# Kernel tuning notes

Measured on AMD Instinct MI355X. Metric: run time of the kernel, lower is better.

The kernel has to match this reference:

```python
import jax, jax.numpy as jnp
import numpy as np

W1 = W2 = W3 = 7  # window size


def _rel_pos_indices(w1, w2, w3):
    # Static relative-position index table, matching the torch buffer.
    g = np.stack(np.meshgrid(np.arange(w1), np.arange(w2), np.arange(w3), indexing='ij'))
    g = g.reshape(3, -1).T                      # (N, 3), N = w1*w2*w3
    rel = g[:, None, :] - g[None, :, :]         # (N, N, 3)
    rel[..., 0] += w1 - 1
    rel[..., 1] += w2 - 1
    rel[..., 2] += w3 - 1
    strides = np.array([(2 * w2 - 1) * (2 * w3 - 1), 2 * w3 - 1, 1])
    return jnp.asarray((rel * strides).sum(-1), dtype=jnp.int32)  # (N, N)


def setup_inputs() -> dict:
    key = jax.random.key(0)
    k1, k2, k3, k4 = jax.random.split(key, 4)
    dim, heads = 256, 8
    x = jax.random.normal(k1, (2, 4, 4, 4, W1, W2, W3, dim), dtype=jnp.float32)
    w_qkv = jax.random.normal(k2, (dim, 3 * dim), dtype=jnp.float32) * (dim ** -0.5)
    w_out = jax.random.normal(k3, (dim, dim), dtype=jnp.float32) * (dim ** -0.5)
    n_rel = (2 * W1 - 1) * (2 * W2 - 1) * (2 * W3 - 1)  # 2197
    rel_bias_table = jax.random.normal(k4, (n_rel, heads), dtype=jnp.float32) * 0.02
    return {"x": x, "w_qkv": w_qkv, "w_out": w_out, "rel_bias_table": rel_bias_table}


def reference(x, w_qkv, w_out, rel_bias_table):
    b, gx, gy, gz, w1, w2, w3, d = x.shape
    heads = rel_bias_table.shape[1]
    dh = d // heads
    scale = dh ** -0.5
    n = w1 * w2 * w3
    B = b * gx * gy * gz

    xf = x.reshape(B, n, d)
    qkv = xf @ w_qkv                             # (B, n, 3d)
    q, k, v = jnp.split(qkv, 3, axis=-1)

    def to_heads(t):
        return t.reshape(B, n, heads, dh).transpose(0, 2, 1, 3)  # (B, h, n, dh)

    q, k, v = to_heads(q), to_heads(k), to_heads(v)

    rel_idx = _rel_pos_indices(w1, w2, w3)                       # (n, n)
    bias = rel_bias_table[rel_idx].transpose(2, 0, 1)            # (h, n, n)

    logits = jnp.einsum('bhnd,bhmd->bhnm', q, k) * scale + bias[None]
    attn = jax.nn.softmax(logits, axis=-1)
    ctx = jnp.einsum('bhnm,bhmd->bhnd', attn, v)                 # (B, h, n, dh)

    out = ctx.transpose(0, 2, 1, 3).reshape(B, n, d) @ w_out     # (B, n, d)
    return out.reshape(b, gx, gy, gz, w1, w2, w3, d)
```

## Files before the change

kernel.cpp:

```cpp
#include <hip/hip_runtime.h>
#include <math.h>

using f16   = _Float16;
using f16x4 = __attribute__((ext_vector_type(4))) _Float16;
using f16x8 = __attribute__((ext_vector_type(8))) _Float16;
using f32x4 = __attribute__((ext_vector_type(4))) float;

#define NW    343
#define NWP   352
#define VTP   356
#define HEADS 8
#define MTOT  43904
#define LOG2E 1.4426950408889634f
#define QSC   (0.17677669529663687f * 1.4426950408889634f)

typedef const __attribute__((address_space(1))) unsigned int* gp1_t;
typedef __attribute__((address_space(3))) unsigned int* lp3_t;
__device__ __forceinline__ void gload_lds16(const void* g, void* l) {
    __builtin_amdgcn_global_load_lds((gp1_t)g, (lp3_t)l, 16, 0, 0);
}

__global__ void cvt_x(const float* __restrict__ x, f16* __restrict__ xb) {
    int id = blockIdx.x * 256 + threadIdx.x;
    float4 v = *(const float4*)(x + id * 4);
    f16x4 o = { (f16)v.x, (f16)v.y, (f16)v.z, (f16)v.w };
    *(f16x4*)(xb + id * 4) = o;
}

__global__ void cvt_wT(const float* __restrict__ W, f16* __restrict__ WT,
                       int N, int scaleN, float sc) {
    int id = blockIdx.x * 256 + threadIdx.x;
    int n = id >> 8, k = id & 255;
    float v = W[k * N + n];
    if (n < scaleN) v *= sc;
    WT[n * 256 + k] = (f16)v;
}

__global__ void bias_k(const float* __restrict__ tab, float* __restrict__ bp) {
    int id = blockIdx.x * 256 + threadIdx.x;
    int h = id / (NWP * NWP);
    int rem = id - h * NWP * NWP;
    int i = rem / NWP, j = rem - (rem / NWP) * NWP;
    float v;
    if (j >= NW) v = -1e30f;
    else if (i >= NW) v = 0.f;
    else {
        int a1 = i / 49, a2 = (i / 7) % 7, a3 = i % 7;
        int b1 = j / 49, b2 = (j / 7) % 7, b3 = j % 7;
        int idx = (a1 - b1 + 6) * 169 + (a2 - b2 + 6) * 13 + (a3 - b3 + 6);
        v = tab[idx * 8 + h] * LOG2E;
    }
    bp[id] = v;
}

template<bool OUT_F32>
__launch_bounds__(256)
__global__ void gemm_k(const f16* __restrict__ A, const f16* __restrict__ Bt,
                       void* __restrict__ Cp, int N) {
    __shared__ f16 As[128 * 32];
    __shared__ f16 Bs[128 * 32];
    const int m0 = blockIdx.x * 128;
    const int n0 = blockIdx.y * 128;
    const int t = threadIdx.x;
    const int wave = t >> 6, lane = t & 63;
    const int q = lane >> 4, c = lane & 15;
    const int wm = (wave >> 1) * 64, wn = (wave & 1) * 64;
    const int r0 = t >> 2;
    const int c8 = (t & 3) * 8;

    f32x4 acc[4][4] = {};
#pragma unroll
    for (int ks = 0; ks < 256; ks += 32) {
        gload_lds16(&A[(size_t)(m0 + r0) * 256 + ks + c8],        &As[r0 * 32 + c8]);
        gload_lds16(&A[(size_t)(m0 + r0 + 64) * 256 + ks + c8],   &As[(r0 + 64) * 32 + c8]);
        gload_lds16(&Bt[(size_t)(n0 + r0) * 256 + ks + c8],       &Bs[r0 * 32 + c8]);
        gload_lds16(&Bt[(size_t)(n0 + r0 + 64) * 256 + ks + c8],  &Bs[(r0 + 64) * 32 + c8]);
        __syncthreads();
        f16x8 af[4], bf[4];
#pragma unroll
        for (int a = 0; a < 4; a++) af[a] = *(const f16x8*)&As[(wm + a * 16 + c) * 32 + q * 8];
#pragma unroll
        for (int b = 0; b < 4; b++) bf[b] = *(const f16x8*)&Bs[(wn + b * 16 + c) * 32 + q * 8];
#pragma unroll
        for (int a = 0; a < 4; a++)
#pragma unroll
            for (int b = 0; b < 4; b++)
                acc[a][b] = __builtin_amdgcn_mfma_f32_16x16x32_f16(af[a], bf[b], acc[a][b], 0, 0, 0);
        __syncthreads();
    }
#pragma unroll
    for (int a = 0; a < 4; a++)
#pragma unroll
        for (int b = 0; b < 4; b++) {
            int row0 = m0 + wm + a * 16 + q * 4;
            int col = n0 + wn + b * 16 + c;
#pragma unroll
            for (int r = 0; r < 4; r++) {
                float v = acc[a][b][r];
                if (OUT_F32) ((float*)Cp)[(size_t)(row0 + r) * N + col] = v;
                else         ((f16*)Cp)[(size_t)(row0 + r) * N + col] = (f16)v;
            }
        }
}

__launch_bounds__(512)
__global__ void attn_k(const f16* __restrict__ qkv, const float* __restrict__ biasP,
                       f16* __restrict__ ctx) {
    const int w = blockIdx.x >> 3;
    const int h = blockIdx.x & 7;
    __shared__ f16 Ks[NWP * 32];
    __shared__ f16 Vt[32 * VTP];
    const int t = threadIdx.x;
    const size_t base = (size_t)(w * NW) * 768;

    for (int u = t; u < NWP * 4; u += 512) {
        int row = u >> 2, un = u & 3;
        uint4 val;
        if (row < NW) val = *(const uint4*)&qkv[base + (size_t)row * 768 + 256 + h * 32 + un * 8];
        else { val.x = val.y = val.z = val.w = 0u; }
        *(uint4*)&Ks[row * 32 + un * 8] = val;
    }
    for (int u = t; u < NWP * 4; u += 512) {
        int row = u >> 2, un = u & 3;
        if (row < NW) {
            uint4 val = *(const uint4*)&qkv[base + (size_t)row * 768 + 512 + h * 32 + un * 8];
            const f16* pv = (const f16*)&val;
#pragma unroll
            for (int e = 0; e < 8; e++) Vt[(un * 8 + e) * VTP + row] = pv[e];
        } else {
#pragma unroll
            for (int e = 0; e < 8; e++) Vt[(un * 8 + e) * VTP + row] = (f16)0.f;
        }
    }
    __syncthreads();

    const int wave = t >> 6, lane = t & 63;
    const int q = lane >> 4, c = lane & 15;
    const float* biasH = biasP + (size_t)h * NWP * NWP;

    for (int qt = wave; qt < NWP / 16; qt += 8) {
        const int iq = qt * 16 + c;
        const int iqc = iq < NW ? iq : NW - 1;
        f16x8 qf = *(const f16x8*)&qkv[base + (size_t)iqc * 768 + h * 32 + q * 8];
        const float* brow = biasH + (size_t)iq * NWP;

        f32x4 o0 = {0.f, 0.f, 0.f, 0.f}, o1 = {0.f, 0.f, 0.f, 0.f};
        float lsum = 0.f;
#pragma unroll
        for (int jt = 0; jt < NWP / 16; jt++) {
            const int jb = jt * 16;
            f16x8 kf = *(const f16x8*)&Ks[(jb + c) * 32 + q * 8];
            f32x4 z = {0.f, 0.f, 0.f, 0.f};
            f32x4 s = __builtin_amdgcn_mfma_f32_16x16x32_f16(kf, qf, z, 0, 0, 0);
            f32x4 b4 = *(const f32x4*)&brow[jb + q * 4];
            float p0 = __builtin_amdgcn_exp2f(s[0] + b4[0]);
            float p1 = __builtin_amdgcn_exp2f(s[1] + b4[1]);
            float p2 = __builtin_amdgcn_exp2f(s[2] + b4[2]);
            float p3 = __builtin_amdgcn_exp2f(s[3] + b4[3]);
            lsum += (p0 + p1) + (p2 + p3);
            f16x4 pf = { (f16)p0, (f16)p1, (f16)p2, (f16)p3 };
            f16x4 v0 = *(const f16x4*)&Vt[c * VTP + jb + q * 4];
            f16x4 v1 = *(const f16x4*)&Vt[(16 + c) * VTP + jb + q * 4];
            o0 = __builtin_amdgcn_mfma_f32_16x16x16f16(v0, pf, o0, 0, 0, 0);
            o1 = __builtin_amdgcn_mfma_f32_16x16x16f16(v1, pf, o1, 0, 0, 0);
        }
        lsum += __shfl_xor(lsum, 16);
        lsum += __shfl_xor(lsum, 32);

        if (iq < NW) {
            float inv = 1.f / lsum;
            size_t ob = (size_t)(w * NW + iq) * 256 + h * 32;
            f16x4 s0 = { (f16)(o0[0] * inv), (f16)(o0[1] * inv),
                         (f16)(o0[2] * inv), (f16)(o0[3] * inv) };
            f16x4 s1 = { (f16)(o1[0] * inv), (f16)(o1[1] * inv),
                         (f16)(o1[2] * inv), (f16)(o1[3] * inv) };
            *(f16x4*)&ctx[ob + q * 4] = s0;
            *(f16x4*)&ctx[ob + 16 + q * 4] = s1;
        }
    }
}

extern "C" void kernel_launch(void* const* d_in, const int* in_sizes, int n_in,
                              void* d_out, int out_size, void* d_ws, size_t ws_size,
                              hipStream_t stream) {
    const float* x    = (const float*)d_in[0];
    const float* wqkv = (const float*)d_in[1];
    const float* wout = (const float*)d_in[2];
    const float* tab  = (const float*)d_in[3];

    char* ws = (char*)d_ws;
    size_t off = 0;
    f16*   xb     = (f16*)(ws + off);   off += (size_t)MTOT * 256 * 2;
    f16*   wqkvT  = (f16*)(ws + off);   off += (size_t)768 * 256 * 2;
    f16*   woutT  = (f16*)(ws + off);   off += (size_t)256 * 256 * 2;
    float* biasP  = (float*)(ws + off); off += (size_t)8 * NWP * NWP * 4;
    f16*   qkvb   = (f16*)(ws + off);   off += (size_t)MTOT * 768 * 2;
    f16*   ctxb   = (f16*)(ws + off);   off += (size_t)MTOT * 256 * 2;
    if (ws_size < off) return;

    cvt_x <<<MTOT * 256 / 1024, 256, 0, stream>>>(x, xb);
    cvt_wT<<<768, 256, 0, stream>>>(wqkv, wqkvT, 768, 256, QSC);
    cvt_wT<<<256, 256, 0, stream>>>(wout, woutT, 256, 0, 1.f);
    bias_k<<<8 * NWP * NWP / 256, 256, 0, stream>>>(tab, biasP);
    gemm_k<false><<<dim3(MTOT / 128, 768 / 128), 256, 0, stream>>>(xb, wqkvT, qkvb, 768);
    attn_k<<<128 * HEADS, 512, 0, stream>>>(qkvb, biasP, ctxb);
    gemm_k<true><<<dim3(MTOT / 128, 256 / 128), 256, 0, stream>>>(ctxb, woutT, d_out, 256);
}
```

Measured before the change: 236.0 us.

## Merge prep kernels, widen GEMM K-tile with swizzle, pad K LDS, split attention accumulators

Three small setup kernels become one launch. The GEMM now stages 64-wide K tiles with an XOR-style swizzle that avoids LDS bank conflicts, which halves the barrier count, and it sets an occupancy hint in launch bounds. In attention, the K rows in LDS are padded to 40, the bias is folded into the QK MFMA accumulator input, and the loop alternates between two accumulator sets to shorten dependency chains. The larger LDS tiles and extra accumulators add register and LDS pressure, which may cost occupancy.

```diff
diff --git a/kernel.cpp b/kernel.cpp
--- a/kernel.cpp
+++ b/kernel.cpp
@@ -8,6 +8,7 @@
 
 #define NW    343
 #define NWP   352
+#define KSP   40
 #define VTP   356
 #define HEADS 8
 #define MTOT  43904
@@ -27,65 +28,81 @@
     *(f16x4*)(xb + id * 4) = o;
 }
 
-__global__ void cvt_wT(const float* __restrict__ W, f16* __restrict__ WT,
-                       int N, int scaleN, float sc) {
-    int id = blockIdx.x * 256 + threadIdx.x;
-    int n = id >> 8, k = id & 255;
-    float v = W[k * N + n];
-    if (n < scaleN) v *= sc;
-    WT[n * 256 + k] = (f16)v;
-}
-
-__global__ void bias_k(const float* __restrict__ tab, float* __restrict__ bp) {
-    int id = blockIdx.x * 256 + threadIdx.x;
-    int h = id / (NWP * NWP);
-    int rem = id - h * NWP * NWP;
-    int i = rem / NWP, j = rem - (rem / NWP) * NWP;
-    float v;
-    if (j >= NW) v = -1e30f;
-    else if (i >= NW) v = 0.f;
-    else {
-        int a1 = i / 49, a2 = (i / 7) % 7, a3 = i % 7;
-        int b1 = j / 49, b2 = (j / 7) % 7, b3 = j % 7;
-        int idx = (a1 - b1 + 6) * 169 + (a2 - b2 + 6) * 13 + (a3 - b3 + 6);
-        v = tab[idx * 8 + h] * LOG2E;
-    }
-    bp[id] = v;
+__global__ void prep_k(const float* __restrict__ wqkv, const float* __restrict__ wout,
+                       const float* __restrict__ tab,
+                       f16* __restrict__ wqkvT, f16* __restrict__ woutT,
+                       float* __restrict__ bp) {
+    int b = blockIdx.x, t = threadIdx.x;
+    if (b < 768) {
+        float v = wqkv[t * 768 + b];
+        if (b < 256) v *= QSC;
+        wqkvT[b * 256 + t] = (f16)v;
+    } else if (b < 1024) {
+        int n = b - 768;
+        woutT[n * 256 + t] = (f16)wout[t * 256 + n];
+    } else {
+        int id = (b - 1024) * 256 + t;
+        int h = id / (NWP * NWP);
+        int rem = id - h * NWP * NWP;
+        int i = rem / NWP, j = rem - (rem / NWP) * NWP;
+        float v;
+        if (j >= NW) v = -1e30f;
+        else if (i >= NW) v = 0.f;
+        else {
+            int a1 = i / 49, a2 = (i / 7) % 7, a3 = i % 7;
+            int b1 = j / 49, b2 = (j / 7) % 7, b3 = j % 7;
+            int idx = (a1 - b1 + 6) * 169 + (a2 - b2 + 6) * 13 + (a3 - b3 + 6);
+            v = tab[idx * 8 + h] * LOG2E;
+        }
+        bp[id] = v;
+    }
 }
 
 template<bool OUT_F32>
-__launch_bounds__(256)
+__launch_bounds__(256, 3)
 __global__ void gemm_k(const f16* __restrict__ A, const f16* __restrict__ Bt,
                        void* __restrict__ Cp, int N) {
-    __shared__ f16 As[128 * 32];
-    __shared__ f16 Bs[128 * 32];
+    __shared__ f16 As[128 * 64];
+    __shared__ f16 Bs[128 * 64];
     const int m0 = blockIdx.x * 128;
     const int n0 = blockIdx.y * 128;
     const int t = threadIdx.x;
     const int wave = t >> 6, lane = t & 63;
     const int q = lane >> 4, c = lane & 15;
     const int wm = (wave >> 1) * 64, wn = (wave & 1) * 64;
-    const int r0 = t >> 2;
-    const int c8 = (t & 3) * 8;
+    const int sr = t >> 3;
+    const int sb = t & 7;
 
     f32x4 acc[4][4] = {};
 #pragma unroll
-    for (int ks = 0; ks < 256; ks += 32) {
-        gload_lds16(&A[(size_t)(m0 + r0) * 256 + ks + c8],        &As[r0 * 32 + c8]);
-        gload_lds16(&A[(size_t)(m0 + r0 + 64) * 256 + ks + c8],   &As[(r0 + 64) * 32 + c8]);
-        gload_lds16(&Bt[(size_t)(n0 + r0) * 256 + ks + c8],       &Bs[r0 * 32 + c8]);
-        gload_lds16(&Bt[(size_t)(n0 + r0 + 64) * 256 + ks + c8],  &Bs[(r0 + 64) * 32 + c8]);
+    for (int ks = 0; ks < 256; ks += 64) {
+#pragma unroll
+        for (int j = 0; j < 4; j++) {
+            int row = j * 32 + sr;
+            int gb = (sb - row) & 7;
+            gload_lds16(&A[(size_t)(m0 + row) * 256 + ks + gb * 8], &As[row * 64 + sb * 8]);
+            gload_lds16(&Bt[(size_t)(n0 + row) * 256 + ks + gb * 8], &Bs[row * 64 + sb * 8]);
+        }
         __syncthreads();
-        f16x8 af[4], bf[4];
-#pragma unroll
-        for (int a = 0; a < 4; a++) af[a] = *(const f16x8*)&As[(wm + a * 16 + c) * 32 + q * 8];
-#pragma unroll
-        for (int b = 0; b < 4; b++) bf[b] = *(const f16x8*)&Bs[(wn + b * 16 + c) * 32 + q * 8];
-#pragma unroll
-        for (int a = 0; a < 4; a++)
-#pragma unroll
-            for (int b = 0; b < 4; b++)
-                acc[a][b] = __builtin_amdgcn_mfma_f32_16x16x32_f16(af[a], bf[b], acc[a][b], 0, 0, 0);
+#pragma unroll
+        for (int ko = 0; ko < 2; ko++) {
+            f16x8 af[4], bf[4];
+#pragma unroll
+            for (int a = 0; a < 4; a++) {
+                int row = wm + a * 16 + c;
+                af[a] = *(const f16x8*)&As[row * 64 + ((ko * 4 + q + row) & 7) * 8];
+            }
+#pragma unroll
+            for (int b = 0; b < 4; b++) {
+                int row = wn + b * 16 + c;
+                bf[b] = *(const f16x8*)&Bs[row * 64 + ((ko * 4 + q + row) & 7) * 8];
+            }
+#pragma unroll
+            for (int a = 0; a < 4; a++)
+#pragma unroll
+                for (int b = 0; b < 4; b++)
+                    acc[a][b] = __builtin_amdgcn_mfma_f32_16x16x32_f16(af[a], bf[b], acc[a][b], 0, 0, 0);
+        }
         __syncthreads();
     }
 #pragma unroll
@@ -103,12 +120,12 @@
         }
 }
 
-__launch_bounds__(512)
+__launch_bounds__(512, 4)
 __global__ void attn_k(const f16* __restrict__ qkv, const float* __restrict__ biasP,
                        f16* __restrict__ ctx) {
     const int w = blockIdx.x >> 3;
     const int h = blockIdx.x & 7;
-    __shared__ f16 Ks[NWP * 32];
+    __shared__ f16 Ks[NWP * KSP];
     __shared__ f16 Vt[32 * VTP];
     const int t = threadIdx.x;
     const size_t base = (size_t)(w * NW) * 768;
@@ -118,7 +135,7 @@
         uint4 val;
         if (row < NW) val = *(const uint4*)&qkv[base + (size_t)row * 768 + 256 + h * 32 + un * 8];
         else { val.x = val.y = val.z = val.w = 0u; }
-        *(uint4*)&Ks[row * 32 + un * 8] = val;
+        *(uint4*)&Ks[row * KSP + un * 8] = val;
     }
     for (int u = t; u < NWP * 4; u += 512) {
         int row = u >> 2, un = u & 3;
@@ -144,36 +161,55 @@
         f16x8 qf = *(const f16x8*)&qkv[base + (size_t)iqc * 768 + h * 32 + q * 8];
         const float* brow = biasH + (size_t)iq * NWP;
 
-        f32x4 o0 = {0.f, 0.f, 0.f, 0.f}, o1 = {0.f, 0.f, 0.f, 0.f};
-        float lsum = 0.f;
-#pragma unroll
-        for (int jt = 0; jt < NWP / 16; jt++) {
-            const int jb = jt * 16;
-            f16x8 kf = *(const f16x8*)&Ks[(jb + c) * 32 + q * 8];
-            f32x4 z = {0.f, 0.f, 0.f, 0.f};
-            f32x4 s = __builtin_amdgcn_mfma_f32_16x16x32_f16(kf, qf, z, 0, 0, 0);
-            f32x4 b4 = *(const f32x4*)&brow[jb + q * 4];
-            float p0 = __builtin_amdgcn_exp2f(s[0] + b4[0]);
-            float p1 = __builtin_amdgcn_exp2f(s[1] + b4[1]);
-            float p2 = __builtin_amdgcn_exp2f(s[2] + b4[2]);
-            float p3 = __builtin_amdgcn_exp2f(s[3] + b4[3]);
-            lsum += (p0 + p1) + (p2 + p3);
-            f16x4 pf = { (f16)p0, (f16)p1, (f16)p2, (f16)p3 };
-            f16x4 v0 = *(const f16x4*)&Vt[c * VTP + jb + q * 4];
-            f16x4 v1 = *(const f16x4*)&Vt[(16 + c) * VTP + jb + q * 4];
-            o0 = __builtin_amdgcn_mfma_f32_16x16x16f16(v0, pf, o0, 0, 0, 0);
-            o1 = __builtin_amdgcn_mfma_f32_16x16x16f16(v1, pf, o1, 0, 0, 0);
-        }
+        f32x4 o0a = {0.f,0.f,0.f,0.f}, o1a = {0.f,0.f,0.f,0.f};
+        f32x4 o0b = {0.f,0.f,0.f,0.f}, o1b = {0.f,0.f,0.f,0.f};
+        float lsa = 0.f, lsb = 0.f;
+#pragma unroll
+        for (int jp = 0; jp < NWP / 32; jp++) {
+            {
+                const int jb = (2 * jp) * 16;
+                f16x8 kf = *(const f16x8*)&Ks[(jb + c) * KSP + q * 8];
+                f32x4 b4 = *(const f32x4*)&brow[jb + q * 4];
+                f32x4 s = __builtin_amdgcn_mfma_f32_16x16x32_f16(kf, qf, b4, 0, 0, 0);
+                float p0 = __builtin_amdgcn_exp2f(s[0]);
+                float p1 = __builtin_amdgcn_exp2f(s[1]);
+                float p2 = __builtin_amdgcn_exp2f(s[2]);
+                float p3 = __builtin_amdgcn_exp2f(s[3]);
+                lsa += (p0 + p1) + (p2 + p3);
+                f16x4 pf = { (f16)p0, (f16)p1, (f16)p2, (f16)p3 };
+                f16x4 v0 = *(const f16x4*)&Vt[c * VTP + jb + q * 4];
+                f16x4 v1 = *(const f16x4*)&Vt[(16 + c) * VTP + jb + q * 4];
+                o0a = __builtin_amdgcn_mfma_f32_16x16x16f16(v0, pf, o0a, 0, 0, 0);
+                o1a = __builtin_amdgcn_mfma_f32_16x16x16f16(v1, pf, o1a, 0, 0, 0);
+            }
+            {
+                const int jb = (2 * jp + 1) * 16;
+                f16x8 kf = *(const f16x8*)&Ks[(jb + c) * KSP + q * 8];
+                f32x4 b4 = *(const f32x4*)&brow[jb + q * 4];
+                f32x4 s = __builtin_amdgcn_mfma_f32_16x16x32_f16(kf, qf, b4, 0, 0, 0);
+                float p0 = __builtin_amdgcn_exp2f(s[0]);
+                float p1 = __builtin_amdgcn_exp2f(s[1]);
+                float p2 = __builtin_amdgcn_exp2f(s[2]);
+                float p3 = __builtin_amdgcn_exp2f(s[3]);
+                lsb += (p0 + p1) + (p2 + p3);
+                f16x4 pf = { (f16)p0, (f16)p1, (f16)p2, (f16)p3 };
+                f16x4 v0 = *(const f16x4*)&Vt[c * VTP + jb + q * 4];
+                f16x4 v1 = *(const f16x4*)&Vt[(16 + c) * VTP + jb + q * 4];
+                o0b = __builtin_amdgcn_mfma_f32_16x16x16f16(v0, pf, o0b, 0, 0, 0);
+                o1b = __builtin_amdgcn_mfma_f32_16x16x16f16(v1, pf, o1b, 0, 0, 0);
+            }
+        }
+        float lsum = lsa + lsb;
         lsum += __shfl_xor(lsum, 16);
         lsum += __shfl_xor(lsum, 32);
 
         if (iq < NW) {
             float inv = 1.f / lsum;
             size_t ob = (size_t)(w * NW + iq) * 256 + h * 32;
-            f16x4 s0 = { (f16)(o0[0] * inv), (f16)(o0[1] * inv),
-                         (f16)(o0[2] * inv), (f16)(o0[3] * inv) };
-            f16x4 s1 = { (f16)(o1[0] * inv), (f16)(o1[1] * inv),
-                         (f16)(o1[2] * inv), (f16)(o1[3] * inv) };
+            f16x4 s0 = { (f16)((o0a[0] + o0b[0]) * inv), (f16)((o0a[1] + o0b[1]) * inv),
+                         (f16)((o0a[2] + o0b[2]) * inv), (f16)((o0a[3] + o0b[3]) * inv) };
+            f16x4 s1 = { (f16)((o1a[0] + o1b[0]) * inv), (f16)((o1a[1] + o1b[1]) * inv),
+                         (f16)((o1a[2] + o1b[2]) * inv), (f16)((o1a[3] + o1b[3]) * inv) };
             *(f16x4*)&ctx[ob + q * 4] = s0;
             *(f16x4*)&ctx[ob + 16 + q * 4] = s1;
         }
@@ -199,9 +235,7 @@
     if (ws_size < off) return;
 
     cvt_x <<<MTOT * 256 / 1024, 256, 0, stream>>>(x, xb);
-    cvt_wT<<<768, 256, 0, stream>>>(wqkv, wqkvT, 768, 256, QSC);
-    cvt_wT<<<256, 256, 0, stream>>>(wout, woutT, 256, 0, 1.f);
-    bias_k<<<8 * NWP * NWP / 256, 256, 0, stream>>>(tab, biasP);
+    prep_k<<<1024 + 8 * NWP * NWP / 256, 256, 0, stream>>>(wqkv, wout, tab, wqkvT, woutT, biasP);
     gemm_k<false><<<dim3(MTOT / 128, 768 / 128), 256, 0, stream>>>(xb, wqkvT, qkvb, 768);
     attn_k<<<128 * HEADS, 512, 0, stream>>>(qkvb, biasP, ctxb);
     gemm_k<true><<<dim3(MTOT / 128, 256 / 128), 256, 0, stream>>>(ctxb, woutT, d_out, 256);
```

Result: slower. 324.7 us (+37.6%).
